# Kernel tuning notes

Measured on AMD Instinct MI355X. Metric: run time of the kernel, lower is better.

Reference implementation:

```python
import jax, jax.numpy as jnp
import numpy as np

OBS_LEN = 20
IN_DIM = 64
HID_DIM = 128
BATCH = 65536


def setup_inputs() -> dict:
    key = jax.random.key(0)
    ks = jax.random.split(key, 9)
    s_emb = 1.0 / np.sqrt(2.0)
    s_lstm = 1.0 / np.sqrt(HID_DIM)
    return {
        "obs_goal": jax.random.normal(ks[0], (OBS_LEN, BATCH, 2), dtype=jnp.float32),
        "h0": jax.random.normal(ks[1], (BATCH, HID_DIM), dtype=jnp.float32),
        "c0": jax.random.normal(ks[2], (BATCH, HID_DIM), dtype=jnp.float32),
        "W_emb": jax.random.uniform(ks[3], (IN_DIM, 2), jnp.float32, -s_emb, s_emb),
        "b_emb": jax.random.uniform(ks[4], (IN_DIM,), jnp.float32, -s_emb, s_emb),
        "W_ih": jax.random.uniform(ks[5], (4 * HID_DIM, IN_DIM), jnp.float32, -s_lstm, s_lstm),
        "W_hh": jax.random.uniform(ks[6], (4 * HID_DIM, HID_DIM), jnp.float32, -s_lstm, s_lstm),
        "b_ih": jax.random.uniform(ks[7], (4 * HID_DIM,), jnp.float32, -s_lstm, s_lstm),
        "b_hh": jax.random.uniform(ks[8], (4 * HID_DIM,), jnp.float32, -s_lstm, s_lstm),
    }


def reference(obs_goal, h0, c0, W_emb, b_emb, W_ih, W_hh, b_ih, b_hh):
    # input embedding: [T*B, 2] @ [2, D] -> [T, B, D]
    T, B, _ = obs_goal.shape
    x_emb = (obs_goal.reshape(-1, 2) @ W_emb.T + b_emb).reshape(T, B, IN_DIM)

    def step(carry, x_t):
        h, c = carry
        # gates: [B, 4H], torch LSTMCell chunk order = (i, f, g, o)
        gates = x_t @ W_ih.T + b_ih + h @ W_hh.T + b_hh
        i, f, g, o = jnp.split(gates, 4, axis=-1)
        i = jax.nn.sigmoid(i)
        f = jax.nn.sigmoid(f)
        g = jnp.tanh(g)
        o = jax.nn.sigmoid(o)
        c_new = f * c + i * g
        h_new = o * jnp.tanh(c_new)
        return (h_new, c_new), None

    (h_final, _), _ = jax.lax.scan(step, (h0, c0), x_emb[:OBS_LEN])
    return h_final
```

## Files before the change

### kernel.cpp

```cpp
#include <hip/hip_runtime.h>

#define OBS_T 20
#define HID 128
#define NGATE 512
#define MB 16
#define HSTR 136

typedef __bf16 bf16x8 __attribute__((ext_vector_type(8)));
typedef __bf16 bf16x4 __attribute__((ext_vector_type(4)));
typedef float f32x4 __attribute__((ext_vector_type(4)));
typedef float f32x2 __attribute__((ext_vector_type(2)));

__device__ __forceinline__ float fast_rcp(float x) { return __builtin_amdgcn_rcpf(x); }
#if __has_builtin(__builtin_amdgcn_exp2f)
__device__ __forceinline__ float exp2_hw(float x) { return __builtin_amdgcn_exp2f(x); }
#else
__device__ __forceinline__ float exp2_hw(float x) { return __expf(x * 0.69314718056f); }
#endif
#define LOG2E 1.442695041f

__device__ __host__ __forceinline__ float gate_scale(int q) {
  return (q == 2) ? (-2.0f * LOG2E) : (-LOG2E);
}

__global__ void prep_vec(const float* __restrict__ W_emb, const float* __restrict__ b_emb,
                         const float* __restrict__ W_ih, const float* __restrict__ b_ih,
                         const float* __restrict__ b_hh, float2* __restrict__ wxb) {
  int r = blockIdx.x * blockDim.x + threadIdx.x;
  if (r >= NGATE) return;
  float s0 = 0.f, s1 = 0.f, sb = 0.f;
  for (int d = 0; d < 64; ++d) {
    float w = W_ih[r * 64 + d];
    s0 += w * W_emb[d * 2 + 0];
    s1 += w * W_emb[d * 2 + 1];
    sb += w * b_emb[d];
  }
  int q = r >> 7, j = r & 127;
  float sc = gate_scale(q);
  int np = (j >> 4) * 64 + q * 16 + (j & 15);
  float w0 = s0 * sc, w1 = s1 * sc, bb = (b_ih[r] + b_hh[r] + sb) * sc;
  wxb[0 * NGATE + np] = make_float2(w0, w0);
  wxb[1 * NGATE + np] = make_float2(w1, w1);
  wxb[2 * NGATE + np] = make_float2(bb, bb);
}

__global__ void prep_wp(const float* __restrict__ W_hh, __bf16* __restrict__ Wp) {
  int tid = blockIdx.x * blockDim.x + threadIdx.x;
  int jj = tid & 7;
  int lane = (tid >> 3) & 63;
  int frag = tid >> 9;
  int ks = frag & 3;
  int q = (frag >> 2) & 3;
  int g16 = frag >> 4;
  int cn = lane & 15, quad = lane >> 4;
  int r = q * 128 + g16 * 16 + cn;
  int k = ks * 32 + quad * 8 + jj;
  Wp[tid] = (__bf16)(W_hh[r * 128 + k] * gate_scale(q));
}

__device__ __forceinline__ f32x2 exp2_2(f32x2 v) {
  f32x2 r;
  r.x = exp2_hw(v.x);
  r.y = exp2_hw(v.y);
  return r;
}
__device__ __forceinline__ f32x2 rcp_2(f32x2 v) {
  f32x2 r;
  r.x = fast_rcp(v.x);
  r.y = fast_rcp(v.y);
  return r;
}

__device__ __forceinline__ f32x2 cell_update_pk(f32x2 gi, f32x2 gf, f32x2 gg,
                                                f32x2 go, f32x2& c) {
  f32x2 e_i = exp2_2(gi);
  f32x2 e_f = exp2_2(gf);
  f32x2 e_g = exp2_2(gg);
  f32x2 e_o = exp2_2(go);
  f32x2 a_i = e_i + 1.f;
  f32x2 a_f = e_f + 1.f;
  f32x2 a_g = e_g + 1.f;
  f32x2 bg = 1.f - e_g;
  f32x2 m1 = a_i * a_g;
  f32x2 r = rcp_2(m1 * a_f);
  f32x2 t = c * m1 + bg * a_f;
  c = t * r;
  f32x2 e_c = exp2_2(c * (-2.f * LOG2E));
  f32x2 a_c = e_c + 1.f;
  f32x2 bc = 1.f - e_c;
  return bc * rcp_2((e_o + 1.f) * a_c);
}

#define ACC_INIT(T)                                                            \
  do {                                                                         \
    f32x2 x01 = *(const f32x2*)&obs_sx[(T)][quad * 4];                         \
    f32x2 x23 = *(const f32x2*)&obs_sx[(T)][quad * 4 + 2];                     \
    f32x2 y01 = *(const f32x2*)&obs_sy[(T)][quad * 4];                         \
    f32x2 y23 = *(const f32x2*)&obs_sy[(T)][quad * 4 + 2];                     \
    _Pragma("unroll") for (int q = 0; q < 4; ++q) {                            \
      const int n = wv * 64 + q * 16 + cn;                                     \
      f32x2 w0 = *(const f32x2*)&wxb_s[0][n][0];                               \
      f32x2 w1 = *(const f32x2*)&wxb_s[1][n][0];                               \
      f32x2 b2 = *(const f32x2*)&wxb_s[2][n][0];                               \
      f32x2 lo = y01 * w1 + (x01 * w0 + b2);                                   \
      f32x2 hi = y23 * w1 + (x23 * w0 + b2);                                   \
      acc[q].x = lo.x;                                                         \
      acc[q].y = lo.y;                                                         \
      acc[q].z = hi.x;                                                         \
      acc[q].w = hi.y;                                                         \
    }                                                                          \
  } while (0)

__global__ __launch_bounds__(512, 4) void lstm_fused(
    const float* __restrict__ obs, const float* __restrict__ h0,
    const float* __restrict__ c0, const __bf16* __restrict__ Wp,
    const float* __restrict__ wxbp, float* __restrict__ out, int batch) {
  __shared__ __align__(16) __bf16 hbuf[2][MB][HSTR];
  __shared__ __align__(16) float obs_sx[OBS_T][MB];
  __shared__ __align__(16) float obs_sy[OBS_T][MB];
  __shared__ __align__(16) float wxb_s[3][NGATE][2];

  const int tid = threadIdx.x;
  const int lane = tid & 63;
  const int wv = tid >> 6;
  const int cn = lane & 15;
  const int quad = lane >> 4;
  const int bbase = blockIdx.x * MB;
  const int ju = wv * 16 + cn;

  if (tid < OBS_T * MB) {
    const int t = tid >> 4, row = tid & 15;
    float2 v = ((const float2*)obs)[t * batch + bbase + row];
    obs_sx[t][row] = v.x;
    obs_sy[t][row] = v.y;
  }
  for (int i = tid; i < 768; i += 512)
    ((float4*)wxb_s)[i] = ((const float4*)wxbp)[i];
  {
    int row = tid >> 5, c4 = tid & 31;
    float4 v = ((const float4*)h0)[(bbase + row) * 32 + c4];
    bf16x4 b;
    b.x = (__bf16)v.x; b.y = (__bf16)v.y; b.z = (__bf16)v.z; b.w = (__bf16)v.w;
    *(bf16x4*)&hbuf[0][row][c4 * 4] = b;
  }

  bf16x8 Bf[4][4];
  {
    const bf16x8* wp8 = (const bf16x8*)Wp;
#pragma unroll
    for (int q = 0; q < 4; ++q)
#pragma unroll
      for (int ks = 0; ks < 4; ++ks)
        Bf[ks][q] = wp8[(wv * 16 + q * 4 + ks) * 64 + lane];
  }

  f32x2 cc2[2];
#pragma unroll
  for (int p = 0; p < 2; ++p) {
    cc2[p].x = c0[(bbase + quad * 4 + 2 * p + 0) * HID + ju];
    cc2[p].y = c0[(bbase + quad * 4 + 2 * p + 1) * HID + ju];
  }

  __syncthreads();

  int cur = 0;
#pragma unroll 1
  for (int t = 0; t < OBS_T - 1; ++t) {
    f32x4 acc[4];
    ACC_INIT(t);

#pragma unroll
    for (int ks = 0; ks < 4; ++ks) {
      bf16x8 Av = *(const bf16x8*)&hbuf[cur][cn][ks * 32 + quad * 8];
#pragma unroll
      for (int q = 0; q < 4; ++q)
        acc[q] = __builtin_amdgcn_mfma_f32_16x16x32_bf16(Av, Bf[ks][q], acc[q], 0, 0, 0);
    }

    const int nxt = cur ^ 1;
    __builtin_amdgcn_s_setprio(1);
    {
      f32x2 hlo = cell_update_pk(acc[0].xy, acc[1].xy, acc[2].xy, acc[3].xy, cc2[0]);
      f32x2 hhi = cell_update_pk(acc[0].zw, acc[1].zw, acc[2].zw, acc[3].zw, cc2[1]);
      hbuf[nxt][quad * 4 + 0][ju] = (__bf16)hlo.x;
      hbuf[nxt][quad * 4 + 1][ju] = (__bf16)hlo.y;
      hbuf[nxt][quad * 4 + 2][ju] = (__bf16)hhi.x;
      hbuf[nxt][quad * 4 + 3][ju] = (__bf16)hhi.y;
    }
    __builtin_amdgcn_s_setprio(0);
    __syncthreads();
    cur = nxt;
  }

  {
    f32x4 acc[4];
    ACC_INIT(OBS_T - 1);
#pragma unroll
    for (int ks = 0; ks < 4; ++ks) {
      bf16x8 Av = *(const bf16x8*)&hbuf[cur][cn][ks * 32 + quad * 8];
#pragma unroll
      for (int q = 0; q < 4; ++q)
        acc[q] = __builtin_amdgcn_mfma_f32_16x16x32_bf16(Av, Bf[ks][q], acc[q], 0, 0, 0);
    }
    f32x2 hlo = cell_update_pk(acc[0].xy, acc[1].xy, acc[2].xy, acc[3].xy, cc2[0]);
    f32x2 hhi = cell_update_pk(acc[0].zw, acc[1].zw, acc[2].zw, acc[3].zw, cc2[1]);
    out[(bbase + quad * 4 + 0) * HID + ju] = hlo.x;
    out[(bbase + quad * 4 + 1) * HID + ju] = hlo.y;
    out[(bbase + quad * 4 + 2) * HID + ju] = hhi.x;
    out[(bbase + quad * 4 + 3) * HID + ju] = hhi.y;
  }
}

extern "C" void kernel_launch(void* const* d_in, const int* in_sizes, int n_in,
                              void* d_out, int out_size, void* d_ws, size_t ws_size,
                              hipStream_t stream) {
  const float* obs = (const float*)d_in[0];
  const float* h0 = (const float*)d_in[1];
  const float* c0 = (const float*)d_in[2];
  const float* W_emb = (const float*)d_in[3];
  const float* b_emb = (const float*)d_in[4];
  const float* W_ih = (const float*)d_in[5];
  const float* W_hh = (const float*)d_in[6];
  const float* b_ih = (const float*)d_in[7];
  const float* b_hh = (const float*)d_in[8];
  float* out = (float*)d_out;
  const int batch = in_sizes[1] / HID;

  __bf16* Wp = (__bf16*)d_ws;
  float2* wxb = (float2*)((char*)d_ws + 131072);

  prep_vec<<<2, 256, 0, stream>>>(W_emb, b_emb, W_ih, b_ih, b_hh, wxb);
  prep_wp<<<256, 256, 0, stream>>>(W_hh, Wp);
  lstm_fused<<<batch / MB, 512, 0, stream>>>(obs, h0, c0, Wp, (const float*)wxb, out, batch);
}
```

Baseline: 337.0 us.

## Replace per-step block barrier with fine-grained LDS producer/consumer flags

Removes the __syncthreads at the end of each recurrent step and replaces it with per-wave progress flags in shared memory. Each wave waits only for the two producer waves whose hidden-state columns feed the current k-slice, and it waits on consumer flags before overwriting the double-buffered h. This lets waves drift out of lockstep and overlap the MFMA and gate math across waves. In exchange it adds spin-polling LDS traffic and relies on memory ordering through volatile shared flags and waitcnt, which is subtle to get right.

```diff
diff --git a/kernel.cpp b/kernel.cpp
--- a/kernel.cpp
+++ b/kernel.cpp
@@ -111,6 +111,24 @@
     }                                                                          \
   } while (0)
 
+#define WAIT_PROD(G2, T)                                                       \
+  do {                                                                         \
+    while (true) {                                                             \
+      int v_ = (int)prodf[(G2) + (lane & 1)];                                  \
+      if (__all(v_ >= (T))) break;                                             \
+    }                                                                          \
+    asm volatile("" ::: "memory");                                             \
+  } while (0)
+
+#define WAIT_CONS(T)                                                           \
+  do {                                                                         \
+    while (true) {                                                             \
+      int v_ = (int)consf[lane & 7];                                           \
+      if (__all(v_ >= (T))) break;                                             \
+    }                                                                          \
+    asm volatile("" ::: "memory");                                             \
+  } while (0)
+
 __global__ __launch_bounds__(512, 4) void lstm_fused(
     const float* __restrict__ obs, const float* __restrict__ h0,
     const float* __restrict__ c0, const __bf16* __restrict__ Wp,
@@ -119,6 +137,8 @@
   __shared__ __align__(16) float obs_sx[OBS_T][MB];
   __shared__ __align__(16) float obs_sy[OBS_T][MB];
   __shared__ __align__(16) float wxb_s[3][NGATE][2];
+  __shared__ volatile int prodf[8];
+  __shared__ volatile int consf[8];
 
   const int tid = threadIdx.x;
   const int lane = tid & 63;
@@ -128,6 +148,10 @@
   const int bbase = blockIdx.x * MB;
   const int ju = wv * 16 + cn;
 
+  if (tid < 8) {
+    prodf[tid] = 0;
+    consf[tid] = 0;
+  }
   if (tid < OBS_T * MB) {
     const int t = tid >> 4, row = tid & 15;
     float2 v = ((const float2*)obs)[t * batch + bbase + row];
@@ -163,40 +187,46 @@
 
   __syncthreads();
 
-  int cur = 0;
 #pragma unroll 1
   for (int t = 0; t < OBS_T - 1; ++t) {
+    const int cur = t & 1;
     f32x4 acc[4];
     ACC_INIT(t);
 
 #pragma unroll
     for (int ks = 0; ks < 4; ++ks) {
+      WAIT_PROD(2 * ks, t);
       bf16x8 Av = *(const bf16x8*)&hbuf[cur][cn][ks * 32 + quad * 8];
 #pragma unroll
       for (int q = 0; q < 4; ++q)
         acc[q] = __builtin_amdgcn_mfma_f32_16x16x32_bf16(Av, Bf[ks][q], acc[q], 0, 0, 0);
     }
-
+    asm volatile("s_waitcnt lgkmcnt(0)" ::: "memory");
+    if (lane == 0) consf[wv] = t + 1;
+
+    __builtin_amdgcn_s_setprio(1);
+    f32x2 hlo = cell_update_pk(acc[0].xy, acc[1].xy, acc[2].xy, acc[3].xy, cc2[0]);
+    f32x2 hhi = cell_update_pk(acc[0].zw, acc[1].zw, acc[2].zw, acc[3].zw, cc2[1]);
+    __builtin_amdgcn_s_setprio(0);
+
+    WAIT_CONS(t);
     const int nxt = cur ^ 1;
-    __builtin_amdgcn_s_setprio(1);
-    {
-      f32x2 hlo = cell_update_pk(acc[0].xy, acc[1].xy, acc[2].xy, acc[3].xy, cc2[0]);
-      f32x2 hhi = cell_update_pk(acc[0].zw, acc[1].zw, acc[2].zw, acc[3].zw, cc2[1]);
-      hbuf[nxt][quad * 4 + 0][ju] = (__bf16)hlo.x;
-      hbuf[nxt][quad * 4 + 1][ju] = (__bf16)hlo.y;
-      hbuf[nxt][quad * 4 + 2][ju] = (__bf16)hhi.x;
-      hbuf[nxt][quad * 4 + 3][ju] = (__bf16)hhi.y;
-    }
-    __builtin_amdgcn_s_setprio(0);
-    __syncthreads();
-    cur = nxt;
+    hbuf[nxt][quad * 4 + 0][ju] = (__bf16)hlo.x;
+    hbuf[nxt][quad * 4 + 1][ju] = (__bf16)hlo.y;
+    hbuf[nxt][quad * 4 + 2][ju] = (__bf16)hhi.x;
+    hbuf[nxt][quad * 4 + 3][ju] = (__bf16)hhi.y;
+    asm volatile("s_waitcnt lgkmcnt(0)" ::: "memory");
+    if (lane == 0) prodf[wv] = t + 1;
   }
 
   {
+    const int t = OBS_T - 1;
+    const int cur = t & 1;
     f32x4 acc[4];
-    ACC_INIT(OBS_T - 1);
+    ACC_INIT(t);
 #pragma unroll
     for (int ks = 0; ks < 4; ++ks) {
+      WAIT_PROD(2 * ks, t);
       bf16x8 Av = *(const bf16x8*)&hbuf[cur][cn][ks * 32 + quad * 8];
 #pragma unroll
       for (int q = 0; q < 4; ++q)
```

New measurement: 378.2 us. +12.2%, slower.
